# Performance work log

Measured on AMD Instinct MI355X. Metric: run time of the kernel, lower is better.

## Reference

```python
import jax, jax.numpy as jnp
import numpy as np

EMBED_DIM = 1408
NUM_HEADS = 16
HEAD_DIM = EMBED_DIM // NUM_HEADS  # 88
SCALE = HEAD_DIM ** -0.5


def setup_inputs() -> dict:
    key = jax.random.key(0)
    k0, k1, k2, k3, k4 = jax.random.split(key, 5)
    B, S, D = 16, 577, EMBED_DIM
    hidden_states = jax.random.normal(k0, (B, S, D), dtype=jnp.float32)
    # fused QKV projection: [D, 3D] laid out as [q | k | v]
    w_qkv = jax.random.normal(k1, (D, 3 * D), dtype=jnp.float32) * (D ** -0.5)
    b_qkv = jax.random.normal(k2, (3 * D,), dtype=jnp.float32) * 0.02
    # output projection
    w_proj = jax.random.normal(k3, (D, D), dtype=jnp.float32) * (D ** -0.5)
    b_proj = jax.random.normal(k4, (D,), dtype=jnp.float32) * 0.02
    return {
        "hidden_states": hidden_states,
        "w_qkv": w_qkv,
        "b_qkv": b_qkv,
        "w_proj": w_proj,
        "b_proj": b_proj,
    }


def reference(hidden_states, w_qkv, b_qkv, w_proj, b_proj):
    B, S, D = hidden_states.shape
    H, Hd = NUM_HEADS, HEAD_DIM
    # fused QKV projection, then chunk along last dim (matches .chunk(3, -1))
    qkv = hidden_states @ w_qkv + b_qkv                      # [B, S, 3D]
    q, k, v = jnp.split(qkv, 3, axis=-1)                     # each [B, S, D]
    q = q.reshape(B, S, H, Hd)
    k = k.reshape(B, S, H, Hd)
    v = v.reshape(B, S, H, Hd)
    # scaled dot-product attention (no mask, no dropout at inference)
    scores = jnp.einsum("bqhd,bkhd->bhqk", q, k) * SCALE      # [B, H, S, S]
    probs = jax.nn.softmax(scores, axis=-1)
    out = jnp.einsum("bhqk,bkhd->bqhd", probs, v)             # [B, S, H, Hd]
    out = out.reshape(B, S, D)
    attn_output = out @ w_proj + b_proj                        # [B, S, D]
    return attn_output
```

## Files before the change

### kernel.cpp

```cpp
#include <hip/hip_runtime.h>
#include <cstddef>
#include <cstdint>

#define D_EMB   1408
#define NHEADS  16
#define HD      88
#define BATCH   16
#define SEQ     577
#define M_ROWS  (BATCH * SEQ)
#define N_QKV   (3 * D_EMB)
#define QKL_N   2816
#define SP      640
#define ATT_SCALE 0.10660035817780521f

#define QT 64
#define KT 64

typedef __attribute__((ext_vector_type(8))) short bf16x8;
typedef __attribute__((ext_vector_type(4))) float f32x4;
typedef unsigned short u16;

static __device__ __forceinline__ u16 f2bf(float x) {
  union { float f; unsigned u; } v; v.f = x;
  unsigned r = v.u + 0x7fff + ((v.u >> 16) & 1);
  return (u16)(r >> 16);
}
static __device__ __forceinline__ float bf2f(u16 h) {
  union { unsigned u; float f; } v; v.u = ((unsigned)h) << 16;
  return v.f;
}
static __device__ __forceinline__ void split_hl(float x, u16* hi, u16* lo) {
  u16 h = f2bf(x);
  *hi = h;
  *lo = f2bf(x - bf2f(h));
}

static __device__ __forceinline__ void async16(const u16* g, u16* l) {
  __builtin_amdgcn_global_load_lds(
      (const __attribute__((address_space(1))) unsigned int*)g,
      (__attribute__((address_space(3))) unsigned int*)l, 16, 0, 0);
}

__global__ __launch_bounds__(256)
void split_kernel(const float* __restrict__ X, u16* __restrict__ H,
                  u16* __restrict__ L, int n4) {
  int i = blockIdx.x * 256 + threadIdx.x;
  if (i >= n4) return;
  float4 v = ((const float4*)X)[i];
  ushort4 h, l;
  split_hl(v.x, &h.x, &l.x);
  split_hl(v.y, &h.y, &l.y);
  split_hl(v.z, &h.z, &l.z);
  split_hl(v.w, &h.w, &l.w);
  ((ushort4*)H)[i] = h;
  ((ushort4*)L)[i] = l;
}

__global__ __launch_bounds__(256)
void transpose_split_kernel(const float* __restrict__ W, u16* __restrict__ Th,
                            u16* __restrict__ Tl, int K, int N) {
  __shared__ float tile[32][33];
  const int n0 = blockIdx.x * 32, k0 = blockIdx.y * 32;
  const int tx = threadIdx.x & 31, ty = threadIdx.x >> 5;
#pragma unroll
  for (int i = 0; i < 4; ++i) {
    int k = ty + i * 8;
    tile[k][tx] = W[(size_t)(k0 + k) * N + n0 + tx];
  }
  __syncthreads();
#pragma unroll
  for (int i = 0; i < 4; ++i) {
    int n = ty + i * 8;
    float v = tile[tx][n];
    u16 h, l;
    split_hl(v, &h, &l);
    Th[(size_t)(n0 + n) * K + k0 + tx] = h;
    Tl[(size_t)(n0 + n) * K + k0 + tx] = l;
  }
}

__global__ __launch_bounds__(256)
void vtrans_kernel(const u16* __restrict__ qkvh, u16* __restrict__ vt) {
  __shared__ u16 tile[64][96];
  const int st = blockIdx.x, bh = blockIdx.y;
  const int b = bh >> 4, h = bh & 15;
  const int tid = threadIdx.x;
  const int s0 = st * 64;
  for (int idx = tid; idx < 64 * 22; idx += 256) {
    int j = idx / 22, c4 = (idx % 22) * 4;
    int s = s0 + j;
    ushort4 v = make_ushort4(0, 0, 0, 0);
    if (s < SEQ)
      v = *(const ushort4*)(qkvh + (size_t)(b * SEQ + s) * N_QKV + 2 * D_EMB + h * HD + c4);
    *(ushort4*)&tile[j][c4] = v;
  }
  if (tid < 64) {
    bf16x8 z = {0, 0, 0, 0, 0, 0, 0, 0};
    *(bf16x8*)&tile[tid][88] = z;
  }
  __syncthreads();
  for (int idx = tid; idx < 96 * 8; idx += 256) {
    int d = idx >> 3, c8 = (idx & 7) * 8;
    bf16x8 o;
#pragma unroll
    for (int e = 0; e < 8; ++e) o[e] = (short)tile[c8 + e][d];
    *(bf16x8*)(vt + ((size_t)bh * 96 + d) * SP + s0 + c8) = o;
  }
}

#define KDIM   1408
#define BMT    256
#define BNT    128
#define SLOT_E 24576
#define AS_H   0
#define AS_L   8192
#define BS_H   16384
#define BS_L   20480

#define STAGE(SLOTP, SSN)                                                 \
  {                                                                       \
    const int k0s = (SSN) * 32;                                           \
    u16* Ls = &Lds[SLOTP][0];                                             \
    async16(Ah + srcA0 + k0s, Ls + AS_H + ldsA0);                         \
    async16(Ah + srcA1 + k0s, Ls + AS_H + ldsA1);                         \
    async16(Al + srcA0 + k0s, Ls + AS_L + ldsA0);                         \
    async16(Al + srcA1 + k0s, Ls + AS_L + ldsA1);                         \
    async16(Bh + srcB0 + k0s, Ls + BS_H + ldsB0);                         \
    async16(Bl + srcB0 + k0s, Ls + BS_L + ldsB0);                         \
  }

#define PHASE(SLOT, NXSLOT, SSN, DO_STAGE, VM)                            \
  {                                                                       \
    const u16* Lb = &Lds[SLOT][0];                                        \
    bf16x8 fah[4], fal[4], fbh[4], fbl[4];                                \
    _Pragma("unroll")                                                     \
    for (int i = 0; i < 4; ++i) {                                         \
      fah[i] = *(const bf16x8*)&Lb[AS_H + offA[i]];                       \
      fal[i] = *(const bf16x8*)&Lb[AS_L + offA[i]];                       \
      fbh[i] = *(const bf16x8*)&Lb[BS_H + offB[i]];                       \
      fbl[i] = *(const bf16x8*)&Lb[BS_L + offB[i]];                       \
    }                                                                     \
    if (DO_STAGE) STAGE(NXSLOT, SSN);                                     \
    asm volatile("s_waitcnt vmcnt(" #VM ")" ::: "memory");                \
    __builtin_amdgcn_s_barrier();                                         \
    asm volatile("s_waitcnt lgkmcnt(0)" ::: "memory");                    \
    __builtin_amdgcn_sched_barrier(0);                                    \
    __builtin_amdgcn_s_setprio(1);                                        \
    _Pragma("unroll")                                                     \
    for (int i = 0; i < 4; ++i) {                                         \
      _Pragma("unroll")                                                   \
      for (int j = 0; j < 4; ++j) {                                       \
        acc[i][j] = __builtin_amdgcn_mfma_f32_16x16x32_bf16(fah[i], fbh[j], acc[i][j], 0, 0, 0); \
        acc[i][j] = __builtin_amdgcn_mfma_f32_16x16x32_bf16(fah[i], fbl[j], acc[i][j], 0, 0, 0); \
        acc[i][j] = __builtin_amdgcn_mfma_f32_16x16x32_bf16(fal[i], fbh[j], acc[i][j], 0, 0, 0); \
      }                                                                   \
    }                                                                     \
    __builtin_amdgcn_s_setprio(0);                                        \
    __builtin_amdgcn_s_barrier();                                         \
  }

template <int MODE>
__global__ __launch_bounds__(512)
void gemm8p_kernel(const u16* __restrict__ Ah, const u16* __restrict__ Al,
                   const u16* __restrict__ Bh, const u16* __restrict__ Bl,
                   const float* __restrict__ bias,
                   float* __restrict__ Cf, u16* __restrict__ Ch, u16* __restrict__ Cl,
                   int M, int N, int NX) {
  const int lin  = blockIdx.x;
  const int xcd  = lin & 7;
  const int t    = lin >> 3;
  const int band = xcd + 8 * (t / NX);
  const int bm0  = band * BMT;
  if (bm0 >= M) return;
  const int bn0  = (t % NX) * BNT;

  __shared__ u16 Lds[3][SLOT_E];

  const int tid  = threadIdx.x;
  const int lane = tid & 63;
  const int w    = tid >> 6;
  const int quad = lane >> 4, lc = lane & 15;
  const int wm   = w >> 1, wn = w & 1;

  size_t srcA0, srcA1, srcB0;
  int ldsA0, ldsA1, ldsB0;
  {
    int r0 = tid >> 2, q0 = tid & 3;
    int ra0 = bm0 + r0; if (ra0 > M - 1) ra0 = M - 1;
    srcA0 = (size_t)ra0 * KDIM + (size_t)((q0 ^ ((r0 >> 1) & 3)) * 8);
    ldsA0 = w * 512;
    int r1 = 128 + r0;
    int ra1 = bm0 + r1; if (ra1 > M - 1) ra1 = M - 1;
    srcA1 = (size_t)ra1 * KDIM + (size_t)((q0 ^ ((r1 >> 1) & 3)) * 8);
    ldsA1 = 4096 + w * 512;
    srcB0 = (size_t)(bn0 + r0) * KDIM + (size_t)((q0 ^ ((r0 >> 1) & 3)) * 8);
    ldsB0 = w * 512;
  }

  int offA[4], offB[4];
  {
    const int qphys = quad ^ ((lc >> 1) & 3);
#pragma unroll
    for (int i = 0; i < 4; ++i) {
      offA[i] = (wm * 64 + i * 16 + lc) * 32 + qphys * 8;
      offB[i] = (wn * 64 + i * 16 + lc) * 32 + qphys * 8;
    }
  }

  f32x4 acc[4][4];
#pragma unroll
  for (int i = 0; i < 4; ++i)
#pragma unroll
    for (int j = 0; j < 4; ++j) acc[i][j] = (f32x4){0.f, 0.f, 0.f, 0.f};

  STAGE(0, 0);
  STAGE(1, 1);
  asm volatile("s_waitcnt vmcnt(6)" ::: "memory");
  __builtin_amdgcn_s_barrier();

#pragma unroll 1
  for (int u = 0; u < 14; ++u) {
    const int s = u * 3;
    PHASE(0, 2, s + 2, true, 6);
    PHASE(1, 0, s + 3, true, 6);
    PHASE(2, 1, s + 4, true, 6);
  }
  PHASE(0, 0, 0, false, 0);
  PHASE(1, 0, 0, false, 0);

#pragma unroll
  for (int j = 0; j < 4; ++j) {
    int col = bn0 + wn * 64 + j * 16 + lc;
    float bj = bias[col];
#pragma unroll
    for (int i = 0; i < 4; ++i) {
#pragma unroll
      for (int rg = 0; rg < 4; ++rg) {
        int row = bm0 + wm * 64 + i * 16 + quad * 4 + rg;
        if (row < M) {
          float v = acc[i][j][rg] + bj;
          if (MODE == 0) {
            Cf[(size_t)row * N + col] = v;
          } else {
            u16 hh, ll;
            split_hl(v, &hh, &ll);
            Ch[(size_t)row * N + col] = hh;
            if (col < QKL_N) Cl[(size_t)row * QKL_N + col] = ll;
          }
        }
      }
    }
  }
}

__global__ __launch_bounds__(256)
void attn_kernel2(const u16* __restrict__ qkvh, const u16* __restrict__ qkvl,
                  const u16* __restrict__ vt,
                  u16* __restrict__ outh, u16* __restrict__ outl) {
  __shared__ u16 Khi[KT][104];
  __shared__ u16 Klo[KT][104];
  __shared__ u16 Vs[96][72];
  __shared__ u16 Pb[QT][72];

  const int tid  = threadIdx.x;
  const int lane = tid & 63;
  const int wv   = tid >> 6;
  const int quad = lane >> 4;
  const int lc   = lane & 15;

  const int qt = blockIdx.x, h = blockIdx.y, b = blockIdx.z;
  const int q0 = qt * QT;

  if (tid < KT) {
    bf16x8 z = {0, 0, 0, 0, 0, 0, 0, 0};
    *(bf16x8*)&Khi[tid][88] = z;
    *(bf16x8*)&Klo[tid][88] = z;
  }

  bf16x8 qh[3], ql[3];
  {
    const bf16x8 z = {0, 0, 0, 0, 0, 0, 0, 0};
    int qrow = q0 + wv * 16 + lc;
    bool qv = qrow < SEQ;
    size_t bh_ = (size_t)(b * SEQ + (qv ? qrow : 0));
#pragma unroll
    for (int ks = 0; ks < 3; ++ks) {
      if (!qv || (ks == 2 && quad == 3)) {
        qh[ks] = z; ql[ks] = z;
      } else {
        qh[ks] = *(const bf16x8*)(qkvh + bh_ * N_QKV + h * HD + ks * 32 + quad * 8);
        ql[ks] = *(const bf16x8*)(qkvl + bh_ * QKL_N + h * HD + ks * 32 + quad * 8);
      }
    }
  }

  float mrow[4], lrow[4];
#pragma unroll
  for (int r = 0; r < 4; ++r) { mrow[r] = -INFINITY; lrow[r] = 0.f; }
  f32x4 oacc[6];
#pragma unroll
  for (int nn = 0; nn < 6; ++nn) oacc[nn] = (f32x4){0.f, 0.f, 0.f, 0.f};

  const u16* vsrc = vt + (size_t)(b * 16 + h) * 96 * SP;

  for (int kt = 0; kt < SP / KT; ++kt) {
    const int k0 = kt * KT;
    __syncthreads();

    for (int idx = tid; idx < KT * 22; idx += 256) {
      int j = idx / 22, c4 = (idx % 22) * 4;
      int s = k0 + j;
      ushort4 kh = make_ushort4(0, 0, 0, 0), kl = make_ushort4(0, 0, 0, 0);
      if (s < SEQ) {
        size_t rb = (size_t)(b * SEQ + s);
        kh = *(const ushort4*)(qkvh + rb * N_QKV + D_EMB + h * HD + c4);
        kl = *(const ushort4*)(qkvl + rb * QKL_N + D_EMB + h * HD + c4);
      }
      *(ushort4*)&Khi[j][c4] = kh;
      *(ushort4*)&Klo[j][c4] = kl;
    }
    for (int idx = tid; idx < 96 * 8; idx += 256) {
      int d = idx >> 3, c8 = (idx & 7) * 8;
      *(bf16x8*)&Vs[d][c8] = *(const bf16x8*)(vsrc + (size_t)d * SP + k0 + c8);
    }
    __syncthreads();

    f32x4 sc[4];
#pragma unroll
    for (int t = 0; t < 4; ++t) {
      f32x4 a = (f32x4){0.f, 0.f, 0.f, 0.f};
#pragma unroll
      for (int ks = 0; ks < 3; ++ks) {
        bf16x8 kh = *(const bf16x8*)&Khi[t * 16 + lc][ks * 32 + quad * 8];
        bf16x8 kl = *(const bf16x8*)&Klo[t * 16 + lc][ks * 32 + quad * 8];
        a = __builtin_amdgcn_mfma_f32_16x16x32_bf16(qh[ks], kh, a, 0, 0, 0);
        a = __builtin_amdgcn_mfma_f32_16x16x32_bf16(qh[ks], kl, a, 0, 0, 0);
        a = __builtin_amdgcn_mfma_f32_16x16x32_bf16(ql[ks], kh, a, 0, 0, 0);
      }
      sc[t] = a;
    }
#pragma unroll
    for (int t = 0; t < 4; ++t) {
      bool valid = (k0 + t * 16 + lc) < SEQ;
#pragma unroll
      for (int r = 0; r < 4; ++r)
        sc[t][r] = valid ? sc[t][r] * ATT_SCALE : -INFINITY;
    }

    float alpha[4];
#pragma unroll
    for (int r = 0; r < 4; ++r) {
      float v = fmaxf(fmaxf(sc[0][r], sc[1][r]), fmaxf(sc[2][r], sc[3][r]));
      v = fmaxf(v, __shfl_xor(v, 1));
      v = fmaxf(v, __shfl_xor(v, 2));
      v = fmaxf(v, __shfl_xor(v, 4));
      v = fmaxf(v, __shfl_xor(v, 8));
      float mnew = fmaxf(mrow[r], v);
      alpha[r] = expf(mrow[r] - mnew);
      mrow[r] = mnew;
      float s = 0.f;
#pragma unroll
      for (int t = 0; t < 4; ++t) {
        float p = expf(sc[t][r] - mnew);
        sc[t][r] = p;
        s += p;
      }
      s += __shfl_xor(s, 1);
      s += __shfl_xor(s, 2);
      s += __shfl_xor(s, 4);
      s += __shfl_xor(s, 8);
      lrow[r] = lrow[r] * alpha[r] + s;
    }
#pragma unroll
    for (int t = 0; t < 4; ++t)
#pragma unroll
      for (int r = 0; r < 4; ++r)
        Pb[wv * 16 + quad * 4 + r][t * 16 + lc] = f2bf(sc[t][r]);
#pragma unroll
    for (int nn = 0; nn < 6; ++nn)
#pragma unroll
      for (int r = 0; r < 4; ++r) oacc[nn][r] *= alpha[r];
    __syncthreads();

    bf16x8 p0 = *(const bf16x8*)&Pb[wv * 16 + lc][quad * 8];
    bf16x8 p1 = *(const bf16x8*)&Pb[wv * 16 + lc][32 + quad * 8];
#pragma unroll
    for (int nn = 0; nn < 6; ++nn) {
      bf16x8 v0 = *(const bf16x8*)&Vs[nn * 16 + lc][quad * 8];
      bf16x8 v1 = *(const bf16x8*)&Vs[nn * 16 + lc][32 + quad * 8];
      oacc[nn] = __builtin_amdgcn_mfma_f32_16x16x32_bf16(p0, v0, oacc[nn], 0, 0, 0);
      oacc[nn] = __builtin_amdgcn_mfma_f32_16x16x32_bf16(p1, v1, oacc[nn], 0, 0, 0);
    }
  }

#pragma unroll
  for (int r = 0; r < 4; ++r) {
    int s = q0 + wv * 16 + quad * 4 + r;
    if (s < SEQ) {
      float inv = 1.f / lrow[r];
      size_t base = (size_t)(b * SEQ + s) * D_EMB + h * HD;
#pragma unroll
      for (int nn = 0; nn < 6; ++nn) {
        int d = nn * 16 + lc;
        if (d < HD) {
          float v = oacc[nn][r] * inv;
          u16 hh, ll;
          split_hl(v, &hh, &ll);
          outh[base + d] = hh;
          outl[base + d] = ll;
        }
      }
    }
  }
}

extern "C" void kernel_launch(void* const* d_in, const int* in_sizes, int n_in,
                              void* d_out, int out_size, void* d_ws, size_t ws_size,
                              hipStream_t stream) {
  const float* hs    = (const float*)d_in[0];
  const float* wqkv  = (const float*)d_in[1];
  const float* bqkv  = (const float*)d_in[2];
  const float* wproj = (const float*)d_in[3];
  const float* bproj = (const float*)d_in[4];
  float* out = (float*)d_out;

  u16* qkvH = (u16*)d_ws;
  u16* qkvL = qkvH + (size_t)M_ROWS * N_QKV;
  u16* hsH  = qkvL + (size_t)M_ROWS * QKL_N;
  u16* hsL  = hsH + (size_t)M_ROWS * D_EMB;
  u16* vt   = hsL + (size_t)M_ROWS * D_EMB;
  u16* wtH  = vt;
  u16* wtL  = wtH + (size_t)N_QKV * D_EMB;
  u16* attnH = hsH;
  u16* attnL = hsL;

  {
    int n4 = (M_ROWS * D_EMB) / 4;
    split_kernel<<<(n4 + 255) / 256, 256, 0, stream>>>(hs, hsH, hsL, n4);
  }
  {
    dim3 g(N_QKV / 32, D_EMB / 32);
    transpose_split_kernel<<<g, 256, 0, stream>>>(wqkv, wtH, wtL, D_EMB, N_QKV);
  }
  {
    gemm8p_kernel<1><<<33 * 40, 512, 0, stream>>>(hsH, hsL, wtH, wtL, bqkv,
                                                  nullptr, qkvH, qkvL,
                                                  M_ROWS, N_QKV, 33);
  }
  {
    dim3 g(SP / 64, BATCH * NHEADS);
    vtrans_kernel<<<g, 256, 0, stream>>>(qkvH, vt);
  }
  {
    dim3 g(SP / QT, NHEADS, BATCH);
    attn_kernel2<<<g, 256, 0, stream>>>(qkvH, qkvL, vt, attnH, attnL);
  }
  {
    dim3 g(D_EMB / 32, D_EMB / 32);
    transpose_split_kernel<<<g, 256, 0, stream>>>(wproj, wtH, wtL, D_EMB, D_EMB);
  }
  {
    gemm8p_kernel<0><<<11 * 40, 512, 0, stream>>>(attnH, attnL, wtH, wtL, bproj,
                                                  out, nullptr, nullptr,
                                                  M_ROWS, D_EMB, 11);
  }
}
```

Measured before the change: 925.3 us.

## Split GEMM k-step into three sub-phases interleaving LDS reads, staging and MFMA

Each k-step of the split-bf16 GEMM mainloop is broken into three sub-phases. Each sub-phase reads only part of the A/B fragments from LDS, issues one third of the async global-to-LDS copies for the next slot, then runs the MFMAs that need just those fragments. The goal is to overlap LDS reads and global loads with matrix work instead of loading every fragment up front. The trade-off is four barriers per step instead of two, and the vmcnt wait moves to the end of the step, which adds synchronisation overhead and scheduling risk.

Result: faster. 888.6 us (-4.0%).

```diff
diff --git a/kernel.cpp b/kernel.cpp
--- a/kernel.cpp
+++ b/kernel.cpp
@@ -117,45 +117,80 @@
 #define BS_H   16384
 #define BS_L   20480
 
-#define STAGE(SLOTP, SSN)                                                 \
+#define STAGE_A0(SLOTP, SSN)                                              \
   {                                                                       \
     const int k0s = (SSN) * 32;                                           \
     u16* Ls = &Lds[SLOTP][0];                                             \
     async16(Ah + srcA0 + k0s, Ls + AS_H + ldsA0);                         \
+    async16(Al + srcA0 + k0s, Ls + AS_L + ldsA0);                         \
+  }
+#define STAGE_A1(SLOTP, SSN)                                              \
+  {                                                                       \
+    const int k0s = (SSN) * 32;                                           \
+    u16* Ls = &Lds[SLOTP][0];                                             \
     async16(Ah + srcA1 + k0s, Ls + AS_H + ldsA1);                         \
-    async16(Al + srcA0 + k0s, Ls + AS_L + ldsA0);                         \
     async16(Al + srcA1 + k0s, Ls + AS_L + ldsA1);                         \
+  }
+#define STAGE_B(SLOTP, SSN)                                               \
+  {                                                                       \
+    const int k0s = (SSN) * 32;                                           \
+    u16* Ls = &Lds[SLOTP][0];                                             \
     async16(Bh + srcB0 + k0s, Ls + BS_H + ldsB0);                         \
     async16(Bl + srcB0 + k0s, Ls + BS_L + ldsB0);                         \
   }
 
-#define PHASE(SLOT, NXSLOT, SSN, DO_STAGE, VM)                            \
+#define MFMA3(I, J)                                                                               \
+  acc[I][J] = __builtin_amdgcn_mfma_f32_16x16x32_bf16(fah[I], fbh[J], acc[I][J], 0, 0, 0);        \
+  acc[I][J] = __builtin_amdgcn_mfma_f32_16x16x32_bf16(fah[I], fbl[J], acc[I][J], 0, 0, 0);        \
+  acc[I][J] = __builtin_amdgcn_mfma_f32_16x16x32_bf16(fal[I], fbh[J], acc[I][J], 0, 0, 0);
+
+#define PH_SYNC                                                           \
+  __builtin_amdgcn_s_barrier();                                           \
+  asm volatile("s_waitcnt lgkmcnt(0)" ::: "memory");                      \
+  __builtin_amdgcn_sched_barrier(0);
+
+#define SLOT_RUN(PHYS, NXPHYS, SSN, DO_STAGE, VM)                         \
   {                                                                       \
-    const u16* Lb = &Lds[SLOT][0];                                        \
+    const u16* Lb = &Lds[PHYS][0];                                        \
     bf16x8 fah[4], fal[4], fbh[4], fbl[4];                                \
-    _Pragma("unroll")                                                     \
-    for (int i = 0; i < 4; ++i) {                                         \
-      fah[i] = *(const bf16x8*)&Lb[AS_H + offA[i]];                       \
-      fal[i] = *(const bf16x8*)&Lb[AS_L + offA[i]];                       \
-      fbh[i] = *(const bf16x8*)&Lb[BS_H + offB[i]];                       \
-      fbl[i] = *(const bf16x8*)&Lb[BS_L + offB[i]];                       \
-    }                                                                     \
-    if (DO_STAGE) STAGE(NXSLOT, SSN);                                     \
+                                 \
+    fah[0] = *(const bf16x8*)&Lb[AS_H + offA[0]];                         \
+    fah[1] = *(const bf16x8*)&Lb[AS_H + offA[1]];                         \
+    fal[0] = *(const bf16x8*)&Lb[AS_L + offA[0]];                         \
+    fal[1] = *(const bf16x8*)&Lb[AS_L + offA[1]];                         \
+    fbh[0] = *(const bf16x8*)&Lb[BS_H + offB[0]];                         \
+    fbh[1] = *(const bf16x8*)&Lb[BS_H + offB[1]];                         \
+    fbl[0] = *(const bf16x8*)&Lb[BS_L + offB[0]];                         \
+    fbl[1] = *(const bf16x8*)&Lb[BS_L + offB[1]];                         \
+    if (DO_STAGE) STAGE_A0(NXPHYS, SSN);                                  \
+    PH_SYNC                                                               \
+    __builtin_amdgcn_s_setprio(1);                                        \
+    MFMA3(0, 0) MFMA3(0, 1) MFMA3(1, 0) MFMA3(1, 1)                       \
+    __builtin_amdgcn_s_setprio(0);                                        \
+    __builtin_amdgcn_s_barrier();                                         \
+                                 \
+    fbh[2] = *(const bf16x8*)&Lb[BS_H + offB[2]];                         \
+    fbh[3] = *(const bf16x8*)&Lb[BS_H + offB[3]];                         \
+    fbl[2] = *(const bf16x8*)&Lb[BS_L + offB[2]];                         \
+    fbl[3] = *(const bf16x8*)&Lb[BS_L + offB[3]];                         \
+    if (DO_STAGE) STAGE_A1(NXPHYS, SSN);                                  \
+    PH_SYNC                                                               \
+    __builtin_amdgcn_s_setprio(1);                                        \
+    MFMA3(0, 2) MFMA3(0, 3) MFMA3(1, 2) MFMA3(1, 3)                       \
+    __builtin_amdgcn_s_setprio(0);                                        \
+    __builtin_amdgcn_s_barrier();                                         \
+                               \
+    fah[2] = *(const bf16x8*)&Lb[AS_H + offA[2]];                         \
+    fah[3] = *(const bf16x8*)&Lb[AS_H + offA[3]];                         \
+    fal[2] = *(const bf16x8*)&Lb[AS_L + offA[2]];                         \
+    fal[3] = *(const bf16x8*)&Lb[AS_L + offA[3]];                         \
+    if (DO_STAGE) STAGE_B(NXPHYS, SSN);                                   \
+    PH_SYNC                                                               \
+    __builtin_amdgcn_s_setprio(1);                                        \
+    MFMA3(2, 2) MFMA3(2, 3) MFMA3(3, 2) MFMA3(3, 3)                       \
+    MFMA3(2, 0) MFMA3(2, 1) MFMA3(3, 0) MFMA3(3, 1)                       \
+    __builtin_amdgcn_s_setprio(0);                                        \
     asm volatile("s_waitcnt vmcnt(" #VM ")" ::: "memory");                \
-    __builtin_amdgcn_s_barrier();                                         \
-    asm volatile("s_waitcnt lgkmcnt(0)" ::: "memory");                    \
-    __builtin_amdgcn_sched_barrier(0);                                    \
-    __builtin_amdgcn_s_setprio(1);                                        \
-    _Pragma("unroll")                                                     \
-    for (int i = 0; i < 4; ++i) {                                         \
-      _Pragma("unroll")                                                   \
-      for (int j = 0; j < 4; ++j) {                                       \
-        acc[i][j] = __builtin_amdgcn_mfma_f32_16x16x32_bf16(fah[i], fbh[j], acc[i][j], 0, 0, 0); \
-        acc[i][j] = __builtin_amdgcn_mfma_f32_16x16x32_bf16(fah[i], fbl[j], acc[i][j], 0, 0, 0); \
-        acc[i][j] = __builtin_amdgcn_mfma_f32_16x16x32_bf16(fal[i], fbh[j], acc[i][j], 0, 0, 0); \
-      }                                                                   \
-    }                                                                     \
-    __builtin_amdgcn_s_setprio(0);                                        \
     __builtin_amdgcn_s_barrier();                                         \
   }
 
@@ -213,20 +248,20 @@
 #pragma unroll
     for (int j = 0; j < 4; ++j) acc[i][j] = (f32x4){0.f, 0.f, 0.f, 0.f};
 
-  STAGE(0, 0);
-  STAGE(1, 1);
+  STAGE_A0(0, 0); STAGE_A1(0, 0); STAGE_B(0, 0);
+  STAGE_A0(1, 1); STAGE_A1(1, 1); STAGE_B(1, 1);
   asm volatile("s_waitcnt vmcnt(6)" ::: "memory");
   __builtin_amdgcn_s_barrier();
 
 #pragma unroll 1
   for (int u = 0; u < 14; ++u) {
     const int s = u * 3;
-    PHASE(0, 2, s + 2, true, 6);
-    PHASE(1, 0, s + 3, true, 6);
-    PHASE(2, 1, s + 4, true, 6);
-  }
-  PHASE(0, 0, 0, false, 0);
-  PHASE(1, 0, 0, false, 0);
+    SLOT_RUN(0, 2, s + 2, true, 6);
+    SLOT_RUN(1, 0, s + 3, true, 6);
+    SLOT_RUN(2, 1, s + 4, true, 6);
+  }
+  SLOT_RUN(0, 0, 0, false, 0);
+  SLOT_RUN(1, 0, 0, false, 0);
 
 #pragma unroll
   for (int j = 0; j < 4; ++j) {
```

## Shrink GEMM tile to 128x128 with double-buffered LDS and two blocks per CU

Applied to the files above, without the earlier changes.

The split-bf16 GEMM moves from a 256x128 tile with 512 threads and a triple-buffered LDS pipeline to a 128x128 tile with 256 threads and double buffering. Launch bounds now allow two blocks per CU, and the grid doubles to cover the smaller tiles. The goal is more resident blocks to hide latency and better balance across CUs. In exchange, each tile reuses operands less, and each phase now waits for all its loads (vmcnt(0)) before the barrier, which shortens the prefetch distance.

New measurement: 902.7 us. 2.4% less time.

```diff
diff --git a/kernel.cpp b/kernel.cpp
--- a/kernel.cpp
+++ b/kernel.cpp
@@ -109,29 +109,36 @@
 }
 
 #define KDIM   1408
-#define BMT    256
+#define BMT    128
 #define BNT    128
-#define SLOT_E 24576
+#define SLOT_E 16384
 #define AS_H   0
-#define AS_L   8192
-#define BS_H   16384
-#define BS_L   20480
-
-#define STAGE(SLOTP, SSN)                                                 \
+#define AS_L   4096
+#define BS_H   8192
+#define BS_L   12288
+
+#define STG_A(SLOTP, SSN)                                                 \
   {                                                                       \
     const int k0s = (SSN) * 32;                                           \
     u16* Ls = &Lds[SLOTP][0];                                             \
-    async16(Ah + srcA0 + k0s, Ls + AS_H + ldsA0);                         \
-    async16(Ah + srcA1 + k0s, Ls + AS_H + ldsA1);                         \
-    async16(Al + srcA0 + k0s, Ls + AS_L + ldsA0);                         \
-    async16(Al + srcA1 + k0s, Ls + AS_L + ldsA1);                         \
-    async16(Bh + srcB0 + k0s, Ls + BS_H + ldsB0);                         \
-    async16(Bl + srcB0 + k0s, Ls + BS_L + ldsB0);                         \
-  }
-
-#define PHASE(SLOT, NXSLOT, SSN, DO_STAGE, VM)                            \
+    async16(Ah + srcA0 + k0s, Ls + AS_H + ldsD0);                         \
+    async16(Ah + srcA1 + k0s, Ls + AS_H + ldsD1);                         \
+    async16(Al + srcA0 + k0s, Ls + AS_L + ldsD0);                         \
+    async16(Al + srcA1 + k0s, Ls + AS_L + ldsD1);                         \
+  }
+#define STG_B(SLOTP, SSN)                                                 \
   {                                                                       \
-    const u16* Lb = &Lds[SLOT][0];                                        \
+    const int k0s = (SSN) * 32;                                           \
+    u16* Ls = &Lds[SLOTP][0];                                             \
+    async16(Bh + srcB0 + k0s, Ls + BS_H + ldsD0);                         \
+    async16(Bh + srcB1 + k0s, Ls + BS_H + ldsD1);                         \
+    async16(Bl + srcB0 + k0s, Ls + BS_L + ldsD0);                         \
+    async16(Bl + srcB1 + k0s, Ls + BS_L + ldsD1);                         \
+  }
+
+#define SLOT_RUN(PHYS, SSN, DO_STAGE, DO_VM)                              \
+  {                                                                       \
+    const u16* Lb = &Lds[PHYS][0];                                        \
     bf16x8 fah[4], fal[4], fbh[4], fbl[4];                                \
     _Pragma("unroll")                                                     \
     for (int i = 0; i < 4; ++i) {                                         \
@@ -140,9 +147,7 @@
       fbh[i] = *(const bf16x8*)&Lb[BS_H + offB[i]];                       \
       fbl[i] = *(const bf16x8*)&Lb[BS_L + offB[i]];                       \
     }                                                                     \
-    if (DO_STAGE) STAGE(NXSLOT, SSN);                                     \
-    asm volatile("s_waitcnt vmcnt(" #VM ")" ::: "memory");                \
-    __builtin_amdgcn_s_barrier();                                         \
+    if (DO_STAGE) { STG_A(PHYS ^ 1, SSN); STG_B(PHYS ^ 1, SSN); }         \
     asm volatile("s_waitcnt lgkmcnt(0)" ::: "memory");                    \
     __builtin_amdgcn_sched_barrier(0);                                    \
     __builtin_amdgcn_s_setprio(1);                                        \
@@ -156,12 +161,13 @@
       }                                                                   \
     }                                                                     \
     __builtin_amdgcn_s_setprio(0);                                        \
+    if (DO_VM) asm volatile("s_waitcnt vmcnt(0)" ::: "memory");           \
     __builtin_amdgcn_s_barrier();                                         \
   }
 
 template <int MODE>
-__global__ __launch_bounds__(512)
-void gemm8p_kernel(const u16* __restrict__ Ah, const u16* __restrict__ Al,
+__global__ __launch_bounds__(256, 2)
+void gemm2b_kernel(const u16* __restrict__ Ah, const u16* __restrict__ Al,
                    const u16* __restrict__ Bh, const u16* __restrict__ Bl,
                    const float* __restrict__ bias,
                    float* __restrict__ Cf, u16* __restrict__ Ch, u16* __restrict__ Cl,
@@ -174,7 +180,7 @@
   if (bm0 >= M) return;
   const int bn0  = (t % NX) * BNT;
 
-  __shared__ u16 Lds[3][SLOT_E];
+  __shared__ u16 Lds[2][SLOT_E];
 
   const int tid  = threadIdx.x;
   const int lane = tid & 63;
@@ -182,28 +188,30 @@
   const int quad = lane >> 4, lc = lane & 15;
   const int wm   = w >> 1, wn = w & 1;
 
-  size_t srcA0, srcA1, srcB0;
-  int ldsA0, ldsA1, ldsB0;
-  {
-    int r0 = tid >> 2, q0 = tid & 3;
+  size_t srcA0, srcA1, srcB0, srcB1;
+  int ldsD0, ldsD1;
+  {
+    int pi0 = tid,        r0 = pi0 >> 2, q0 = pi0 & 3;
+    int pi1 = 256 + tid,  r1 = pi1 >> 2, q1 = pi1 & 3;
+    int c0 = (q0 ^ ((r0 >> 1) & 3)) * 8;
+    int c1 = (q1 ^ ((r1 >> 1) & 3)) * 8;
     int ra0 = bm0 + r0; if (ra0 > M - 1) ra0 = M - 1;
-    srcA0 = (size_t)ra0 * KDIM + (size_t)((q0 ^ ((r0 >> 1) & 3)) * 8);
-    ldsA0 = w * 512;
-    int r1 = 128 + r0;
     int ra1 = bm0 + r1; if (ra1 > M - 1) ra1 = M - 1;
-    srcA1 = (size_t)ra1 * KDIM + (size_t)((q0 ^ ((r1 >> 1) & 3)) * 8);
-    ldsA1 = 4096 + w * 512;
-    srcB0 = (size_t)(bn0 + r0) * KDIM + (size_t)((q0 ^ ((r0 >> 1) & 3)) * 8);
-    ldsB0 = w * 512;
+    srcA0 = (size_t)ra0 * KDIM + c0;
+    srcA1 = (size_t)ra1 * KDIM + c1;
+    srcB0 = (size_t)(bn0 + r0) * KDIM + c0;
+    srcB1 = (size_t)(bn0 + r1) * KDIM + c1;
+    ldsD0 = w * 512;
+    ldsD1 = 2048 + w * 512;
   }
 
   int offA[4], offB[4];
   {
-    const int qphys = quad ^ ((lc >> 1) & 3);
+    const int qp = quad ^ ((lc >> 1) & 3);
 #pragma unroll
     for (int i = 0; i < 4; ++i) {
-      offA[i] = (wm * 64 + i * 16 + lc) * 32 + qphys * 8;
-      offB[i] = (wn * 64 + i * 16 + lc) * 32 + qphys * 8;
+      offA[i] = (wm * 64 + i * 16 + lc) * 32 + qp * 8;
+      offB[i] = (wn * 64 + i * 16 + lc) * 32 + qp * 8;
     }
   }
 
@@ -213,20 +221,18 @@
 #pragma unroll
     for (int j = 0; j < 4; ++j) acc[i][j] = (f32x4){0.f, 0.f, 0.f, 0.f};
 
-  STAGE(0, 0);
-  STAGE(1, 1);
-  asm volatile("s_waitcnt vmcnt(6)" ::: "memory");
+  STG_A(0, 0);
+  STG_B(0, 0);
+  asm volatile("s_waitcnt vmcnt(0)" ::: "memory");
   __builtin_amdgcn_s_barrier();
 
 #pragma unroll 1
-  for (int u = 0; u < 14; ++u) {
-    const int s = u * 3;
-    PHASE(0, 2, s + 2, true, 6);
-    PHASE(1, 0, s + 3, true, 6);
-    PHASE(2, 1, s + 4, true, 6);
-  }
-  PHASE(0, 0, 0, false, 0);
-  PHASE(1, 0, 0, false, 0);
+  for (int u = 0; u < 21; ++u) {
+    SLOT_RUN(0, 2 * u + 1, true, true);
+    SLOT_RUN(1, 2 * u + 2, true, true);
+  }
+  SLOT_RUN(0, 43, true, true);
+  SLOT_RUN(1, 0, false, false);
 
 #pragma unroll
   for (int j = 0; j < 4; ++j) {
@@ -443,7 +449,7 @@
     transpose_split_kernel<<<g, 256, 0, stream>>>(wqkv, wtH, wtL, D_EMB, N_QKV);
   }
   {
-    gemm8p_kernel<1><<<33 * 40, 512, 0, stream>>>(hsH, hsL, wtH, wtL, bqkv,
+    gemm2b_kernel<1><<<33 * 80, 256, 0, stream>>>(hsH, hsL, wtH, wtL, bqkv,
                                                   nullptr, qkvH, qkvL,
                                                   M_ROWS, N_QKV, 33);
   }
@@ -460,7 +466,7 @@
     transpose_split_kernel<<<g, 256, 0, stream>>>(wproj, wtH, wtL, D_EMB, D_EMB);
   }
   {
-    gemm8p_kernel<0><<<11 * 40, 512, 0, stream>>>(attnH, attnL, wtH, wtL, bproj,
+    gemm2b_kernel<0><<<11 * 80, 256, 0, stream>>>(attnH, attnL, wtH, wtL, bproj,
                                                   out, nullptr, nullptr,
                                                   M_ROWS, D_EMB, 11);
   }
```
